# Performance work log

Hardware: AMD Instinct MI355X
Metric: run time of the kernel (lower is better)

Reference implementation:

```python
import jax, jax.numpy as jnp
import numpy as np
import math

NUM_HEADS = 16
LOGIT_SCALE_MAX = math.log(1.0 / 0.01)  # log(100)
EPS = 1e-12


def _l2norm(x):
    # F.normalize(x, dim=-1): x / max(||x||_2, eps)
    n = jnp.sqrt(jnp.sum(x * x, axis=-1, keepdims=True))
    return x / jnp.maximum(n, EPS)


def setup_inputs() -> dict:
    key = jax.random.key(0)
    ks = jax.random.split(key, 6)
    N, B, C = 1024, 4, 1024
    scale = (C // NUM_HEADS) ** -0.5
    return {
        "query": jax.random.normal(ks[0], (N, B, C), jnp.float32),
        "key": jax.random.normal(ks[1], (N, B, C), jnp.float32),
        "value": jax.random.normal(ks[2], (N, B, C), jnp.float32),
        "in_proj_w": jax.random.normal(ks[3], (3 * C, C), jnp.float32) * scale,
        "in_proj_b": jnp.zeros((3 * C,), jnp.float32),
        "logit_scale": jnp.log(10.0) * jnp.ones((NUM_HEADS, 1, 1), jnp.float32),
        "out_w": jax.random.normal(ks[4], (C, C), jnp.float32) * scale,
        "out_b": jnp.zeros((C,), jnp.float32),
    }


def reference(query, key, value, in_proj_w, in_proj_b, logit_scale, out_w, out_b):
    N, B, C = query.shape
    H = NUM_HEADS
    hd = C // H
    # packed in-projection, split into q/k/v pieces
    w_q, w_k, w_v = jnp.split(in_proj_w, 3, axis=0)
    b_q, b_k, b_v = jnp.split(in_proj_b, 3, axis=0)
    q = query @ w_q.T + b_q          # (N, B, C)
    k = key @ w_k.T + b_k
    v = value @ w_v.T + b_v
    # (N, B, C) -> (B*H, N, hd)
    q = q.reshape(N, B * H, hd).swapaxes(0, 1)
    k = k.reshape(N, B * H, hd).swapaxes(0, 1)
    v = v.reshape(N, B * H, hd).swapaxes(0, 1)
    # cosine-similarity scores with learnable per-head logit scale
    attn = jnp.einsum('bqd,bkd->bqk', _l2norm(q), _l2norm(k))  # (B*H, N, N)
    ls = jnp.exp(jnp.minimum(logit_scale, LOGIT_SCALE_MAX))     # (H,1,1)
    attn = (attn.reshape(B, H, N, N) * ls).reshape(B * H, N, N)
    attn = jax.nn.softmax(attn, axis=-1)
    x = jnp.einsum('bqk,bkd->bqd', attn, v)                     # (B*H, N, hd)
    x = x.swapaxes(0, 1).reshape(N, B, C)
    return x @ out_w.T + out_b
```

## Files before the change

### kernel.cpp

```cpp
#include <hip/hip_runtime.h>


typedef _Float16 f16x8 __attribute__((ext_vector_type(8)));
typedef float    f32x4 __attribute__((ext_vector_type(4)));

#define LOG2E 1.4426950408889634f
#define LOGMAX 4.6051702f

#define GLOAD16(g, l) \
    __builtin_amdgcn_global_load_lds((__attribute__((address_space(1))) void*)(g), \
                                     (__attribute__((address_space(3))) void*)(l), 16, 0, 0)

__device__ __forceinline__ unsigned short f2h(float x) {
    union { _Float16 h; unsigned short u; } cv;
    cv.h = (_Float16)x;
    return cv.u;
}

__global__ __launch_bounds__(256) void cvt_all(
    const float* __restrict__ q, const float* __restrict__ k,
    const float* __restrict__ v, const float* __restrict__ w,
    const float* __restrict__ ow,
    unsigned short* __restrict__ qbf, unsigned short* __restrict__ kbf,
    unsigned short* __restrict__ vbf, unsigned short* __restrict__ wbf,
    unsigned short* __restrict__ owbf)
{
    int b = blockIdx.x;
    const float* src; unsigned short* dst; int idx;
    if      (b < 4096)  { src = q;  dst = qbf;  idx = b; }
    else if (b < 8192)  { src = k;  dst = kbf;  idx = b - 4096; }
    else if (b < 12288) { src = v;  dst = vbf;  idx = b - 8192; }
    else if (b < 15360) { src = w;  dst = wbf;  idx = b - 12288; }
    else                { src = ow; dst = owbf; idx = b - 15360; }
    int i = idx * 256 + threadIdx.x;
    float4 val = ((const float4*)src)[i];
    ushort4 o;
    o.x = f2h(val.x); o.y = f2h(val.y); o.z = f2h(val.z); o.w = f2h(val.w);
    ((ushort4*)dst)[i] = o;
}

__global__ __launch_bounds__(256) void proj_gemm(
    const unsigned short* __restrict__ qbf, const unsigned short* __restrict__ kbf,
    const unsigned short* __restrict__ vbf, const unsigned short* __restrict__ wbf,
    const float* __restrict__ bias, const float* __restrict__ lsc,
    unsigned short* __restrict__ qn, unsigned short* __restrict__ kn,
    unsigned short* __restrict__ vT)
{
    __shared__ __align__(16) unsigned short AsmF[128 * 64];
    __shared__ __align__(16) unsigned short BsmF[128 * 64];
    int tid = threadIdx.x;
    int lane = tid & 63, wave = tid >> 6;
    int lr = lane & 15, lq = lane >> 4;
    int wr = wave >> 1, wc = wave & 1;

    int lin = blockIdx.x;
    int xcd = lin & 7, s = lin >> 3;
    int xt = s & 7, yy = (s >> 3) & 3, z = s >> 5;
    int m0 = (xcd * 4 + yy) * 128, n0 = xt * 128;

    const unsigned short* A = (z == 0) ? qbf : (z == 1) ? kbf : vbf;
    const unsigned short* W = wbf + (size_t)z * 1024 * 1024;

    int rl = lane >> 3;
    int cg = ((lane & 7) ^ rl) << 3;
    const unsigned short* gA = A + (size_t)(m0 + wave * 32 + rl) * 1024 + cg;
    const unsigned short* gB = W + (size_t)(n0 + wave * 32 + rl) * 1024 + cg;
    unsigned short* lA = &AsmF[wave * 32 * 64];
    unsigned short* lB = &BsmF[wave * 32 * 64];

    int swz = lr & 7;
    int c0 = (lq ^ swz) << 3;
    int c1 = ((lq ^ 4) ^ swz) << 3;

    f32x4 acc[4][4];
    for (int i = 0; i < 4; i++) for (int j = 0; j < 4; j++) acc[i][j] = (f32x4){0.f, 0.f, 0.f, 0.f};

    for (int ki = 0; ki < 16; ++ki) {
        for (int j = 0; j < 4; ++j) {
            GLOAD16(gA + ki * 64 + j * 8192, lA + j * 512);
            GLOAD16(gB + ki * 64 + j * 8192, lB + j * 512);
        }
        __syncthreads();
        for (int kc = 0; kc < 2; ++kc) {
            int co = kc ? c1 : c0;
            f16x8 af[4], bfr[4];
            for (int mi = 0; mi < 4; ++mi) af[mi]  = *(const f16x8*)&AsmF[(wr * 64 + mi * 16 + lr) * 64 + co];
            for (int ni = 0; ni < 4; ++ni) bfr[ni] = *(const f16x8*)&BsmF[(wc * 64 + ni * 16 + lr) * 64 + co];
            for (int mi = 0; mi < 4; ++mi)
                for (int ni = 0; ni < 4; ++ni)
                    acc[mi][ni] = __builtin_amdgcn_mfma_f32_16x16x32_f16(af[mi], bfr[ni], acc[mi][ni], 0, 0, 0);
        }
        __syncthreads();
    }

    int h = (n0 >> 6) + wc;
    float bv[4];
    for (int ni = 0; ni < 4; ++ni) bv[ni] = bias[z * 1024 + n0 + wc * 64 + ni * 16 + lr];
    for (int mi = 0; mi < 4; ++mi)
        for (int ni = 0; ni < 4; ++ni)
            for (int r = 0; r < 4; ++r) acc[mi][ni][r] += bv[ni];

    float lsfac = __expf(fminf(lsc[h], LOGMAX)) * LOG2E;

    for (int mi = 0; mi < 4; ++mi)
        for (int r = 0; r < 4; ++r) {
            int row = m0 + wr * 64 + mi * 16 + lq * 4 + r;
            int n = row >> 2, b = row & 3;
            int bh = b * 16 + h;
            if (z < 2) {
                float ss = 0.f;
                for (int ni = 0; ni < 4; ++ni) ss += acc[mi][ni][r] * acc[mi][ni][r];
                for (int off = 1; off < 16; off <<= 1) ss += __shfl_xor(ss, off);
                float scale = 1.0f / fmaxf(sqrtf(ss), 1e-12f);
                if (z == 0) scale *= lsfac;
                unsigned short* dst = (z == 0) ? qn : kn;
                for (int ni = 0; ni < 4; ++ni)
                    dst[(size_t)bh * 65536 + (size_t)n * 64 + ni * 16 + lr] = f2h(acc[mi][ni][r] * scale);
            } else {
                for (int ni = 0; ni < 4; ++ni)
                    vT[(size_t)bh * 65536 + (size_t)(ni * 16 + lr) * 1024 + n] = f2h(acc[mi][ni][r]);
            }
        }
}

__global__ __launch_bounds__(256) void flash_kernel(
    const unsigned short* __restrict__ qn, const unsigned short* __restrict__ kn,
    const unsigned short* __restrict__ vT, const float* __restrict__ lsc,
    unsigned short* __restrict__ xb)
{
    __shared__ __align__(16) unsigned short K_flat[64 * 64];
    __shared__ __align__(16) unsigned short V_flat[64 * 64];
    __shared__ __align__(16) unsigned short P_lds[4][16][72];
    int tid = threadIdx.x;
    int lane = tid & 63, wave = tid >> 6;
    int lr = lane & 15, lq = lane >> 4;

    int lin = blockIdx.x;
    int xcd = lin & 7, s = lin >> 3;
    int qt = s & 15, bh = xcd * 8 + (s >> 4);
    int q0 = qt * 64 + wave * 16;

    float off = __expf(fminf(lsc[bh & 15], LOGMAX)) * LOG2E - 12.0f;

    f16x8 qf[2];
    for (int kc = 0; kc < 2; ++kc)
        qf[kc] = *(const f16x8*)(qn + (size_t)bh * 65536 + (size_t)(q0 + lr) * 64 + kc * 32 + lq * 8);

    int rl = lane >> 3;
    int cg = ((lane & 7) ^ rl) << 3;
    const unsigned short* gK = kn + (size_t)bh * 65536 + (size_t)(wave * 16 + rl) * 64 + cg;
    const unsigned short* gV = vT + (size_t)bh * 65536 + (size_t)(wave * 16 + rl) * 1024 + cg;
    unsigned short* lK = &K_flat[wave * 16 * 64];
    unsigned short* lV = &V_flat[wave * 16 * 64];
    int swz = lr & 7;
    int c0 = (lq ^ swz) << 3;
    int c1 = ((lq ^ 4) ^ swz) << 3;

    f32x4 o[4];
    for (int i = 0; i < 4; i++) o[i] = (f32x4){0.f, 0.f, 0.f, 0.f};
    float lsum = 0.f;

    for (int kt = 0; kt < 16; ++kt) {
        for (int j = 0; j < 2; ++j) {
            GLOAD16(gK + kt * 4096 + j * 512,  lK + j * 512);
            GLOAD16(gV + kt * 64  + j * 8192,  lV + j * 512);
        }
        __syncthreads();

        f32x4 sa[4];
        for (int ct = 0; ct < 4; ++ct) {
            f32x4 a = (f32x4){0.f, 0.f, 0.f, 0.f};
            for (int kc = 0; kc < 2; ++kc) {
                f16x8 kf = *(const f16x8*)&K_flat[(ct * 16 + lr) * 64 + (kc ? c1 : c0)];
                a = __builtin_amdgcn_mfma_f32_16x16x32_f16(kf, qf[kc], a, 0, 0, 0);
            }
            sa[ct] = a;
        }

        for (int ct = 0; ct < 4; ++ct) {
            float p0 = exp2f(sa[ct][0] - off), p1 = exp2f(sa[ct][1] - off);
            float p2 = exp2f(sa[ct][2] - off), p3 = exp2f(sa[ct][3] - off);
            lsum += (p0 + p1) + (p2 + p3);
            ushort4 pw;
            pw.x = f2h(p0); pw.y = f2h(p1); pw.z = f2h(p2); pw.w = f2h(p3);
            *(ushort4*)&P_lds[wave][lr][ct * 16 + lq * 4] = pw;
        }

        f16x8 pf[2];
        for (int kc = 0; kc < 2; ++kc)
            pf[kc] = *(const f16x8*)&P_lds[wave][lr][kc * 32 + lq * 8];
        for (int nt = 0; nt < 4; ++nt)
            for (int kc = 0; kc < 2; ++kc) {
                f16x8 vf = *(const f16x8*)&V_flat[(nt * 16 + lr) * 64 + (kc ? c1 : c0)];
                o[nt] = __builtin_amdgcn_mfma_f32_16x16x32_f16(vf, pf[kc], o[nt], 0, 0, 0);
            }
        __syncthreads();
    }

    lsum += __shfl_xor(lsum, 16);
    lsum += __shfl_xor(lsum, 32);
    float inv = 1.0f / lsum;

    int b = bh >> 4, h = bh & 15;
    for (int nt = 0; nt < 4; ++nt) {
        ushort4 w;
        w.x = f2h(o[nt][0] * inv); w.y = f2h(o[nt][1] * inv);
        w.z = f2h(o[nt][2] * inv); w.w = f2h(o[nt][3] * inv);
        size_t m = (size_t)(q0 + lr) * 4 + b;
        *(ushort4*)(xb + m * 1024 + h * 64 + nt * 16 + lq * 4) = w;
    }
}

__global__ __launch_bounds__(256) void out_gemm(
    const unsigned short* __restrict__ xb, const unsigned short* __restrict__ owbf,
    const float* __restrict__ bias, float* __restrict__ outp)
{
    __shared__ __align__(16) unsigned short AsmF[128 * 64];
    __shared__ __align__(16) unsigned short BsmF[64 * 64];
    int tid = threadIdx.x;
    int lane = tid & 63, wave = tid >> 6;
    int lr = lane & 15, lq = lane >> 4;

    int lin = blockIdx.x;
    int xcd = lin & 7, s = lin >> 3;
    int xt = s & 15, yy = s >> 4;
    int m0 = (xcd * 4 + yy) * 128, n0 = xt * 64;

    int rl = lane >> 3;
    int cg = ((lane & 7) ^ rl) << 3;
    const unsigned short* gA = xb   + (size_t)(m0 + wave * 32 + rl) * 1024 + cg;
    const unsigned short* gB = owbf + (size_t)(n0 + wave * 16 + rl) * 1024 + cg;
    unsigned short* lA = &AsmF[wave * 32 * 64];
    unsigned short* lB = &BsmF[wave * 16 * 64];
    int swz = lr & 7;
    int c0 = (lq ^ swz) << 3;
    int c1 = ((lq ^ 4) ^ swz) << 3;

    f32x4 acc[2][4];
    for (int i = 0; i < 2; i++) for (int j = 0; j < 4; j++) acc[i][j] = (f32x4){0.f, 0.f, 0.f, 0.f};

    for (int ki = 0; ki < 16; ++ki) {
        for (int j = 0; j < 4; ++j)
            GLOAD16(gA + ki * 64 + j * 8192, lA + j * 512);
        for (int j = 0; j < 2; ++j)
            GLOAD16(gB + ki * 64 + j * 8192, lB + j * 512);
        __syncthreads();
        for (int kc = 0; kc < 2; ++kc) {
            int co = kc ? c1 : c0;
            f16x8 af[2], bfr[4];
            for (int mi = 0; mi < 2; ++mi) af[mi]  = *(const f16x8*)&AsmF[(wave * 32 + mi * 16 + lr) * 64 + co];
            for (int ni = 0; ni < 4; ++ni) bfr[ni] = *(const f16x8*)&BsmF[(ni * 16 + lr) * 64 + co];
            for (int mi = 0; mi < 2; ++mi)
                for (int ni = 0; ni < 4; ++ni)
                    acc[mi][ni] = __builtin_amdgcn_mfma_f32_16x16x32_f16(af[mi], bfr[ni], acc[mi][ni], 0, 0, 0);
        }
        __syncthreads();
    }
    for (int mi = 0; mi < 2; ++mi)
        for (int ni = 0; ni < 4; ++ni)
            for (int r = 0; r < 4; ++r) {
                int row = m0 + wave * 32 + mi * 16 + lq * 4 + r;
                int col = n0 + ni * 16 + lr;
                outp[(size_t)row * 1024 + col] = acc[mi][ni][r] + bias[col];
            }
}

extern "C" void kernel_launch(void* const* d_in, const int* in_sizes, int n_in,
                              void* d_out, int out_size, void* d_ws, size_t ws_size,
                              hipStream_t stream) {
    const float* query = (const float*)d_in[0];
    const float* key   = (const float*)d_in[1];
    const float* value = (const float*)d_in[2];
    const float* ipw   = (const float*)d_in[3];
    const float* ipb   = (const float*)d_in[4];
    const float* lsc   = (const float*)d_in[5];
    const float* ow    = (const float*)d_in[6];
    const float* ob    = (const float*)d_in[7];
    float* outp = (float*)d_out;

    char* ws = (char*)d_ws;
    unsigned short* qbf  = (unsigned short*)(ws);
    unsigned short* kbf  = (unsigned short*)(ws + 8388608);
    unsigned short* vbf  = (unsigned short*)(ws + 16777216);
    unsigned short* wbf  = (unsigned short*)(ws + 25165824);
    unsigned short* owbf = (unsigned short*)(ws + 31457280);
    unsigned short* qn   = (unsigned short*)(ws + 33554432);
    unsigned short* kn   = (unsigned short*)(ws + 41943040);
    unsigned short* vT   = (unsigned short*)(ws + 50331648);
    unsigned short* xbuf = (unsigned short*)(ws + 58720256);

    cvt_all<<<16384, 256, 0, stream>>>(query, key, value, ipw, ow,
                                       qbf, kbf, vbf, wbf, owbf);
    proj_gemm<<<768, 256, 0, stream>>>(qbf, kbf, vbf, wbf, ipb, lsc, qn, kn, vT);
    flash_kernel<<<1024, 256, 0, stream>>>(qn, kn, vT, lsc, xbuf);
    out_gemm<<<512, 256, 0, stream>>>(xbuf, owbf, ob, outp);
}
```

Baseline: 212.3 us.

## Process two query groups per wave in flash kernel to reuse K/V tiles

Each block now handles 128 query rows instead of 64, with every wave computing two 16-row groups against the same K and V tiles held in LDS. This halves the grid and the total K/V global-to-LDS traffic, and amortizes each LDS fragment read over two MFMAs. The softmax offset is folded into the MFMA accumulator initial value, which removes a subtraction per score. The cost is more registers per thread and fewer blocks, which lowers parallelism on a large GPU.

```diff
diff --git a/kernel.cpp b/kernel.cpp
--- a/kernel.cpp
+++ b/kernel.cpp
@@ -130,21 +130,24 @@
 {
     __shared__ __align__(16) unsigned short K_flat[64 * 64];
     __shared__ __align__(16) unsigned short V_flat[64 * 64];
-    __shared__ __align__(16) unsigned short P_lds[4][16][72];
+    __shared__ __align__(16) unsigned short P_lds[4][2][16][72];
     int tid = threadIdx.x;
     int lane = tid & 63, wave = tid >> 6;
     int lr = lane & 15, lq = lane >> 4;
 
     int lin = blockIdx.x;
     int xcd = lin & 7, s = lin >> 3;
-    int qt = s & 15, bh = xcd * 8 + (s >> 4);
-    int q0 = qt * 64 + wave * 16;
+    int qt = s & 7, bh = xcd * 8 + (s >> 3);
+    int q0 = qt * 128;
 
     float off = __expf(fminf(lsc[bh & 15], LOGMAX)) * LOG2E - 12.0f;
-
-    f16x8 qf[2];
-    for (int kc = 0; kc < 2; ++kc)
-        qf[kc] = *(const f16x8*)(qn + (size_t)bh * 65536 + (size_t)(q0 + lr) * 64 + kc * 32 + lq * 8);
+    f32x4 initv = (f32x4){-off, -off, -off, -off};
+
+    f16x8 qf[2][2];
+    for (int g = 0; g < 2; ++g)
+        for (int kc = 0; kc < 2; ++kc)
+            qf[g][kc] = *(const f16x8*)(qn + (size_t)bh * 65536 +
+                          (size_t)(q0 + g * 64 + wave * 16 + lr) * 64 + kc * 32 + lq * 8);
 
     int rl = lane >> 3;
     int cg = ((lane & 7) ^ rl) << 3;
@@ -156,9 +159,9 @@
     int c0 = (lq ^ swz) << 3;
     int c1 = ((lq ^ 4) ^ swz) << 3;
 
-    f32x4 o[4];
-    for (int i = 0; i < 4; i++) o[i] = (f32x4){0.f, 0.f, 0.f, 0.f};
-    float lsum = 0.f;
+    f32x4 o[2][4];
+    for (int g = 0; g < 2; ++g) for (int i = 0; i < 4; i++) o[g][i] = (f32x4){0.f, 0.f, 0.f, 0.f};
+    float lsum[2] = {0.f, 0.f};
 
     for (int kt = 0; kt < 16; ++kt) {
         for (int j = 0; j < 2; ++j) {
@@ -167,47 +170,52 @@
         }
         __syncthreads();
 
-        f32x4 sa[4];
+        f32x4 sc[2][4];
         for (int ct = 0; ct < 4; ++ct) {
-            f32x4 a = (f32x4){0.f, 0.f, 0.f, 0.f};
             for (int kc = 0; kc < 2; ++kc) {
                 f16x8 kf = *(const f16x8*)&K_flat[(ct * 16 + lr) * 64 + (kc ? c1 : c0)];
-                a = __builtin_amdgcn_mfma_f32_16x16x32_f16(kf, qf[kc], a, 0, 0, 0);
-            }
-            sa[ct] = a;
-        }
-
-        for (int ct = 0; ct < 4; ++ct) {
-            float p0 = exp2f(sa[ct][0] - off), p1 = exp2f(sa[ct][1] - off);
-            float p2 = exp2f(sa[ct][2] - off), p3 = exp2f(sa[ct][3] - off);
-            lsum += (p0 + p1) + (p2 + p3);
-            ushort4 pw;
-            pw.x = f2h(p0); pw.y = f2h(p1); pw.z = f2h(p2); pw.w = f2h(p3);
-            *(ushort4*)&P_lds[wave][lr][ct * 16 + lq * 4] = pw;
-        }
-
-        f16x8 pf[2];
-        for (int kc = 0; kc < 2; ++kc)
-            pf[kc] = *(const f16x8*)&P_lds[wave][lr][kc * 32 + lq * 8];
+                for (int g = 0; g < 2; ++g)
+                    sc[g][ct] = __builtin_amdgcn_mfma_f32_16x16x32_f16(
+                        kf, qf[g][kc], kc == 0 ? initv : sc[g][ct], 0, 0, 0);
+            }
+        }
+
+        for (int g = 0; g < 2; ++g)
+            for (int ct = 0; ct < 4; ++ct) {
+                float p0 = exp2f(sc[g][ct][0]), p1 = exp2f(sc[g][ct][1]);
+                float p2 = exp2f(sc[g][ct][2]), p3 = exp2f(sc[g][ct][3]);
+                lsum[g] += (p0 + p1) + (p2 + p3);
+                ushort4 pw;
+                pw.x = f2h(p0); pw.y = f2h(p1); pw.z = f2h(p2); pw.w = f2h(p3);
+                *(ushort4*)&P_lds[wave][g][lr][ct * 16 + lq * 4] = pw;
+            }
+
+        f16x8 pf[2][2];
+        for (int g = 0; g < 2; ++g)
+            for (int kc = 0; kc < 2; ++kc)
+                pf[g][kc] = *(const f16x8*)&P_lds[wave][g][lr][kc * 32 + lq * 8];
         for (int nt = 0; nt < 4; ++nt)
             for (int kc = 0; kc < 2; ++kc) {
                 f16x8 vf = *(const f16x8*)&V_flat[(nt * 16 + lr) * 64 + (kc ? c1 : c0)];
-                o[nt] = __builtin_amdgcn_mfma_f32_16x16x32_f16(vf, pf[kc], o[nt], 0, 0, 0);
+                for (int g = 0; g < 2; ++g)
+                    o[g][nt] = __builtin_amdgcn_mfma_f32_16x16x32_f16(vf, pf[g][kc], o[g][nt], 0, 0, 0);
             }
         __syncthreads();
     }
 
-    lsum += __shfl_xor(lsum, 16);
-    lsum += __shfl_xor(lsum, 32);
-    float inv = 1.0f / lsum;
-
     int b = bh >> 4, h = bh & 15;
-    for (int nt = 0; nt < 4; ++nt) {
-        ushort4 w;
-        w.x = f2h(o[nt][0] * inv); w.y = f2h(o[nt][1] * inv);
-        w.z = f2h(o[nt][2] * inv); w.w = f2h(o[nt][3] * inv);
-        size_t m = (size_t)(q0 + lr) * 4 + b;
-        *(ushort4*)(xb + m * 1024 + h * 64 + nt * 16 + lq * 4) = w;
+    for (int g = 0; g < 2; ++g) {
+        float ls = lsum[g];
+        ls += __shfl_xor(ls, 16);
+        ls += __shfl_xor(ls, 32);
+        float inv = 1.0f / ls;
+        size_t m = (size_t)(q0 + g * 64 + wave * 16 + lr) * 4 + b;
+        for (int nt = 0; nt < 4; ++nt) {
+            ushort4 w;
+            w.x = f2h(o[g][nt][0] * inv); w.y = f2h(o[g][nt][1] * inv);
+            w.z = f2h(o[g][nt][2] * inv); w.w = f2h(o[g][nt][3] * inv);
+            *(ushort4*)(xb + m * 1024 + h * 64 + nt * 16 + lq * 4) = w;
+        }
     }
 }
 
@@ -292,6 +300,6 @@
     cvt_all<<<16384, 256, 0, stream>>>(query, key, value, ipw, ow,
                                        qbf, kbf, vbf, wbf, owbf);
     proj_gemm<<<768, 256, 0, stream>>>(qbf, kbf, vbf, wbf, ipb, lsc, qn, kn, vT);
-    flash_kernel<<<1024, 256, 0, stream>>>(qn, kn, vT, lsc, xbuf);
+    flash_kernel<<<512, 256, 0, stream>>>(qn, kn, vT, lsc, xbuf);
     out_gemm<<<512, 256, 0, stream>>>(xbuf, owbf, ob, outp);
 }
```

New measurement: 207.2 us. -2.4%, faster.
